# Performance work log

Measured on AMD Instinct MI355X. Metric: run time of the kernel, lower is better.

Reference implementation:

```python
import jax, jax.numpy as jnp
import numpy as np

LN_EPS = 1e-5


def setup_inputs() -> dict:
    key = jax.random.key(0)
    ks = jax.random.split(key, 10)
    B, T, D, K = 32, 1024, 512, 3
    enc = jax.random.normal(ks[0], (B, T, D), jnp.float32)
    dur = jax.random.randint(ks[1], (B, T), 0, 7, jnp.int32)
    s = 0.02
    return {
        "encoder_output": enc,
        "duration_target": dur,
        "conv1_w": jax.random.normal(ks[2], (K, D, D), jnp.float32) * s,  # HIO layout
        "conv1_b": jnp.zeros((D,), jnp.float32),
        "ln1_w": jnp.ones((D,), jnp.float32),
        "ln1_b": jnp.zeros((D,), jnp.float32),
        "conv2_w": jax.random.normal(ks[3], (K, D, D), jnp.float32) * s,
        "conv2_b": jnp.zeros((D,), jnp.float32),
        "ln2_w": jnp.ones((D,), jnp.float32),
        "ln2_b": jnp.zeros((D,), jnp.float32),
        "lin_w": jax.random.normal(ks[4], (D, 1), jnp.float32) * s,
        "lin_b": jnp.zeros((1,), jnp.float32),
        "max_len": 4096,
    }


def _conv_relu(x, w, b):
    # x: [B,T,D], w: [K, D_in, D_out] ('HIO'), 'SAME' padding == torch padding=1 for k=3
    y = jax.lax.conv_general_dilated(
        x, w, window_strides=(1,), padding="SAME",
        dimension_numbers=("NHC", "HIO", "NHC"))
    return jax.nn.relu(y + b)


def _layernorm(x, g, b):
    mu = jnp.mean(x, axis=-1, keepdims=True)
    var = jnp.mean(jnp.square(x - mu), axis=-1, keepdims=True)
    return (x - mu) * jax.lax.rsqrt(var + LN_EPS) * g + b


def reference(encoder_output, duration_target, conv1_w, conv1_b, ln1_w, ln1_b,
              conv2_w, conv2_b, ln2_w, ln2_b, lin_w, lin_b, max_len):
    B, T, D = encoder_output.shape
    # duration predictor: conv -> relu -> LN -> conv -> relu -> LN -> linear
    h = _layernorm(_conv_relu(encoder_output, conv1_w, conv1_b), ln1_w, ln1_b)
    h = _layernorm(_conv_relu(h, conv2_w, conv2_b), ln2_w, ln2_b)
    duration_predictor_output = (h @ lin_w + lin_b)[..., 0]  # [B,T]

    # training path: expand by duration_target via fused gather with cumulative offsets
    cum = jnp.cumsum(duration_target, axis=1)          # [B,T]
    pos = jnp.arange(max_len, dtype=jnp.int32)         # [L]
    # src index for output frame j: first t with cum[t] > j
    idx = jax.vmap(lambda c: jnp.searchsorted(c, pos, side="right"))(cum)  # [B,L]
    valid = pos[None, :] < cum[:, -1:]                  # [B,L]
    idx = jnp.minimum(idx, T - 1)
    expanded = jnp.take_along_axis(encoder_output, idx[:, :, None], axis=1)
    expanded = expanded * valid[:, :, None].astype(encoder_output.dtype)
    return expanded, duration_predictor_output
```

## Files before the change

kernel.cpp:

```cpp
#include <hip/hip_runtime.h>
#include <hip/hip_bf16.h>

#define BB 32
#define TT 1024
#define DD 512
#define LL 4096
#define KDIM 1536
#define TP 1026
#define ROWS (BB * TT)
#define NT (KDIM / 32)

typedef __attribute__((ext_vector_type(8))) short short8;
typedef __attribute__((ext_vector_type(8))) unsigned short ushort8;
typedef __attribute__((ext_vector_type(4))) float floatx4;

__device__ __forceinline__ unsigned short f2bf(float f) {
  unsigned int u = __builtin_bit_cast(unsigned int, f);
  u += 0x7FFF + ((u >> 16) & 1);
  return (unsigned short)(u >> 16);
}

#define GLOAD_LDS16(g, l)                                          \
  __builtin_amdgcn_global_load_lds(                                \
      (const __attribute__((address_space(1))) void*)(g),          \
      (__attribute__((address_space(3))) void*)(l), 16, 0, 0)

#define PAD_BLKS ((BB * TP) / 4)
#define W0 (PAD_BLKS + 16)
#define C0 (W0 + 384)
#define PREP_BLKS (C0 + 32)

__global__ __launch_bounds__(256) void prep_kernel(
    const float* __restrict__ X, unsigned short* __restrict__ Xp,
    unsigned short* __restrict__ Hp,
    const float* __restrict__ W1, unsigned short* __restrict__ Wt1,
    const float* __restrict__ W2, unsigned short* __restrict__ Wt2,
    const int* __restrict__ dur, int* __restrict__ cum,
    int* __restrict__ idx) {
  __shared__ float tile[64][65];
  const int tid = threadIdx.x;
  const int lane = tid & 63;

  if (blockIdx.x >= C0) {
    int* ls = reinterpret_cast<int*>(tile);
    const int b = blockIdx.x - C0;
    int4 v = reinterpret_cast<const int4*>(dur + b * TT)[tid];
    const int s0 = v.x, s1 = s0 + v.y, s2 = s1 + v.z, s3 = s2 + v.w;
    ls[tid] = s3;
    __syncthreads();
    for (int off = 1; off < 256; off <<= 1) {
      int x = (tid >= off) ? ls[tid - off] : 0;
      __syncthreads();
      ls[tid] += x;
      __syncthreads();
    }
    const int base = tid ? ls[tid - 1] : 0;
    int4 o = {base + s0, base + s1, base + s2, base + s3};
    reinterpret_cast<int4*>(cum + b * TT)[tid] = o;
    int* ib = idx + b * LL;
    int st = base;
    const int dv[4] = {v.x, v.y, v.z, v.w};
#pragma unroll
    for (int k = 0; k < 4; ++k) {
      const int e = min(st + dv[k], LL);
      for (int j = st; j < e; ++j) ib[j] = 4 * tid + k;
      st += dv[k];
    }
    return;
  }
  if (blockIdx.x >= W0) {
    const int w = blockIdx.x - W0;
    const int z = w / 192;
    const int rem = w - z * 192;
    const int bx = rem & 7;
    const int by = rem >> 3;
    const float* W = z ? W2 : W1;
    unsigned short* Wt = z ? Wt2 : Wt1;
    const int n0 = bx * 64;
    const int k0 = by * 64;
    const int c = lane;
    const int r4 = tid >> 6;
#pragma unroll
    for (int r = 0; r < 16; ++r)
      tile[r * 4 + r4][c] = W[(long)(k0 + r * 4 + r4) * DD + n0 + c];
    __syncthreads();
#pragma unroll
    for (int r = 0; r < 16; ++r)
      Wt[(long)(n0 + r * 4 + r4) * KDIM + k0 + c] = f2bf(tile[c][r * 4 + r4]);
    return;
  }
  if (blockIdx.x >= PAD_BLKS) {
    const int hid = (blockIdx.x - PAD_BLKS) * 4 + (tid >> 6);
    const int b = hid >> 1;
    const long r = (long)b * TP + ((hid & 1) ? (TP - 1) : 0);
    *reinterpret_cast<ushort8*>(Hp + r * DD + lane * 8) = (ushort8)0;
    return;
  }
  const int row = blockIdx.x * 4 + (tid >> 6);
  const int b  = row / TP;
  const int pr = row - b * TP;
  ushort8* o = reinterpret_cast<ushort8*>(Xp + (long)row * DD + lane * 8);
  ushort8 v;
  if (pr == 0 || pr == TP - 1) {
    v = (ushort8)0;
  } else {
    const float* p = X + ((long)(b * TT + pr - 1)) * DD + lane * 8;
    float4 a = *reinterpret_cast<const float4*>(p);
    float4 c = *reinterpret_cast<const float4*>(p + 4);
    v[0] = f2bf(a.x); v[1] = f2bf(a.y); v[2] = f2bf(a.z); v[3] = f2bf(a.w);
    v[4] = f2bf(c.x); v[5] = f2bf(c.y); v[6] = f2bf(c.z); v[7] = f2bf(c.w);
  }
  *o = v;
}

template <int LAYER>
__global__ __launch_bounds__(1024, 4) void fused_conv_ln_kernel(
    const unsigned short* __restrict__ Xp, const unsigned short* __restrict__ Wt,
    const float* __restrict__ bias, const float* __restrict__ g,
    const float* __restrict__ be, const float* __restrict__ lw,
    const float* __restrict__ lb, unsigned short* __restrict__ Hp,
    float* __restrict__ dpo) {
  __shared__ unsigned short As[3][128 * 32];
  __shared__ unsigned short Bs[3][512 * 32];
  __shared__ float sS[8][128];
  __shared__ float sQ[8][128];
  __shared__ float muL[128];
  __shared__ float rsL[128];

  const int tid  = threadIdx.x;
  const int lane = tid & 63;
  const int wid  = tid >> 6;
  const int srow = lane >> 2;
  const int gchunk = (lane & 3) ^ (srow & 3) ^ ((srow >> 2) & 3);
  const int frow = lane & 15;
  const int quad = lane >> 4;
  const int rdch = quad ^ (frow & 3) ^ ((frow >> 2) & 3);
  const int wm = (wid >> 3) * 64;
  const int wn = (wid & 7) * 64;
  const int wc = wid & 7;

  const int m0 = blockIdx.x * 128;
  const int bA = m0 >> 10;
  const int t0 = m0 & (TT - 1);

  const unsigned short* gA0 =
      Xp + (long)(bA * TP + t0 + (wid & 7) * 16 + srow) * DD + gchunk * 8;
  const int bb0 = (wid < 8) ? wid * 32 : 256 + (wid - 8) * 32;
  const unsigned short* gB0 =
      Wt + (long)(bb0 + srow) * KDIM + gchunk * 8;

  floatx4 acc[4][4];
#pragma unroll
  for (int i = 0; i < 4; ++i)
#pragma unroll
    for (int j = 0; j < 4; ++j) acc[i][j] = (floatx4){0.f, 0.f, 0.f, 0.f};

#define STAGE(bi, kk)                                                         \
  do {                                                                        \
    const int tap_ = (kk) >> 9;                                               \
    const int c0_  = (kk) & 511;                                              \
    if (wid < 8)                                                              \
      GLOAD_LDS16(gA0 + (long)tap_ * DD + c0_, &As[bi][(wid * 16) * 32]);     \
    GLOAD_LDS16(gB0 + (kk),                &Bs[bi][bb0 * 32]);                \
    GLOAD_LDS16(gB0 + (long)16 * KDIM + (kk), &Bs[bi][(bb0 + 16) * 32]);      \
  } while (0)

#define COMPUTE(bi)                                                           \
  do {                                                                        \
    short8 a_[4], b_[4];                                                      \
    _Pragma("unroll")                                                         \
    for (int i = 0; i < 4; ++i)                                               \
      a_[i] = *reinterpret_cast<const short8*>(                               \
          &As[bi][(wm + i * 16 + frow) * 32 + rdch * 8]);                     \
    _Pragma("unroll")                                                         \
    for (int j = 0; j < 4; ++j)                                               \
      b_[j] = *reinterpret_cast<const short8*>(                               \
          &Bs[bi][(wn + j * 16 + frow) * 32 + rdch * 8]);                     \
    _Pragma("unroll")                                                         \
    for (int i = 0; i < 4; ++i)                                               \
      _Pragma("unroll")                                                       \
      for (int j = 0; j < 4; ++j)                                             \
        acc[i][j] = __builtin_amdgcn_mfma_f32_16x16x32_bf16(                  \
            a_[i], b_[j], acc[i][j], 0, 0, 0);                                \
  } while (0)

  STAGE(0, 0);
  STAGE(1, 32);

  int cur = 0;
  int stg = 2;
  for (int t = 0; t < NT - 1; ++t) {
    if (wid < 8) asm volatile("s_waitcnt vmcnt(3)" ::: "memory");
    else         asm volatile("s_waitcnt vmcnt(2)" ::: "memory");
    __builtin_amdgcn_s_barrier();
    __builtin_amdgcn_sched_barrier(0);
    if (t + 2 < NT) STAGE(stg, (t + 2) * 32);
    COMPUTE(cur);
    cur = (cur == 2) ? 0 : cur + 1;
    stg = (stg == 2) ? 0 : stg + 1;
  }
  asm volatile("s_waitcnt vmcnt(0)" ::: "memory");
  __builtin_amdgcn_s_barrier();
  __builtin_amdgcn_sched_barrier(0);
  COMPUTE(cur);
#undef STAGE
#undef COMPUTE

  float bz[4];
#pragma unroll
  for (int j = 0; j < 4; ++j) bz[j] = bias[wn + j * 16 + frow];
#pragma unroll
  for (int i = 0; i < 4; ++i)
#pragma unroll
    for (int j = 0; j < 4; ++j)
#pragma unroll
      for (int r = 0; r < 4; ++r)
        acc[i][j][r] = fmaxf(acc[i][j][r] + bz[j], 0.f);

  float ps[16], pq[16];
#pragma unroll
  for (int i = 0; i < 4; ++i)
#pragma unroll
    for (int r = 0; r < 4; ++r) {
      float s = 0.f, q = 0.f;
#pragma unroll
      for (int j = 0; j < 4; ++j) {
        const float v = acc[i][j][r];
        s += v; q += v * v;
      }
      ps[i * 4 + r] = s; pq[i * 4 + r] = q;
    }
#pragma unroll
  for (int off = 1; off < 16; off <<= 1)
#pragma unroll
    for (int k = 0; k < 16; ++k) {
      ps[k] += __shfl_xor(ps[k], off);
      pq[k] += __shfl_xor(pq[k], off);
    }
  if (frow == 0) {
#pragma unroll
    for (int i = 0; i < 4; ++i)
#pragma unroll
      for (int r = 0; r < 4; ++r) {
        const int row = wm + i * 16 + quad * 4 + r;
        sS[wc][row] = ps[i * 4 + r];
        sQ[wc][row] = pq[i * 4 + r];
      }
  }
  __syncthreads();
  if (tid < 128) {
    float s = 0.f, q = 0.f;
#pragma unroll
    for (int c = 0; c < 8; ++c) { s += sS[c][tid]; q += sQ[c][tid]; }
    const float mu = s * (1.f / DD);
    const float var = q * (1.f / DD) - mu * mu;
    muL[tid] = mu;
    rsL[tid] = rsqrtf(var + 1e-5f);
  }
  __syncthreads();

  float gg[4], bb[4];
#pragma unroll
  for (int j = 0; j < 4; ++j) {
    gg[j] = g[wn + j * 16 + frow];
    bb[j] = be[wn + j * 16 + frow];
  }

  if constexpr (LAYER == 1) {
    unsigned short* Ls = &Bs[0][0];
    const int h = wm >> 6;
#pragma unroll
    for (int ph = 0; ph < 2; ++ph) {
      __syncthreads();
      if (h == ph) {
#pragma unroll
        for (int i = 0; i < 4; ++i)
#pragma unroll
          for (int r = 0; r < 4; ++r) {
            const int row = wm + i * 16 + quad * 4 + r;
            const float mu = muL[row];
            const float rs = rsL[row];
            const int lrow = row - ph * 64;
#pragma unroll
            for (int j = 0; j < 4; ++j) {
              const float v = (acc[i][j][r] - mu) * rs * gg[j] + bb[j];
              Ls[lrow * 520 + wn + j * 16 + frow] = f2bf(v);
            }
          }
      }
      __syncthreads();
      const long gbase = (long)(bA * TP + t0 + ph * 64 + 1) * DD;
#pragma unroll
      for (int it = 0; it < 4; ++it) {
        const int r2 = it * 16 + wid;
        const int cc = lane * 8;
        ushort8 val = *reinterpret_cast<const ushort8*>(&Ls[r2 * 520 + cc]);
        *reinterpret_cast<ushort8*>(&Hp[gbase + (long)r2 * DD + cc]) = val;
      }
    }
  } else {
    float ww[4];
#pragma unroll
    for (int j = 0; j < 4; ++j) ww[j] = lw[wn + j * 16 + frow];
#pragma unroll
    for (int i = 0; i < 4; ++i)
#pragma unroll
      for (int r = 0; r < 4; ++r) {
        const int row = wm + i * 16 + quad * 4 + r;
        const float mu = muL[row];
        const float rs = rsL[row];
        float d = 0.f;
#pragma unroll
        for (int j = 0; j < 4; ++j) {
          const float v = (acc[i][j][r] - mu) * rs * gg[j] + bb[j];
          d += v * ww[j];
        }
#pragma unroll
        for (int off = 1; off < 16; off <<= 1) d += __shfl_xor(d, off);
        if (frow == 0) sS[wc][row] = d;
      }
    __syncthreads();
    if (tid < 128) {
      float s = lb[0];
#pragma unroll
      for (int c = 0; c < 8; ++c) s += sS[c][tid];
      dpo[blockIdx.x * 128 + tid] = s;
    }
  }
}

__global__ __launch_bounds__(512) void gather_kernel(
    const float* __restrict__ X, const int* __restrict__ cum,
    const int* __restrict__ idx, float* __restrict__ out) {
  const long gf = (long)blockIdx.x * 4 + (threadIdx.x >> 7);
  const int tl = threadIdx.x & 127;
  const int b = (int)(gf >> 12);
  const int j = (int)(gf & (LL - 1));
  const int total = cum[b * TT + TT - 1];
  floatx4* o = reinterpret_cast<floatx4*>(out + gf * DD) + tl;
  if (j >= total) {
    *o = (floatx4){0.f, 0.f, 0.f, 0.f};
    return;
  }
  const int lo = idx[b * LL + j];
  const floatx4* src =
      reinterpret_cast<const floatx4*>(X + ((long)b * TT + lo) * DD) + tl;
  *o = *src;
}

extern "C" void kernel_launch(void* const* d_in, const int* in_sizes, int n_in,
                              void* d_out, int out_size, void* d_ws,
                              size_t ws_size, hipStream_t stream) {
  const float* enc = (const float*)d_in[0];
  const int* dur   = (const int*)d_in[1];
  const float* w1  = (const float*)d_in[2];
  const float* b1  = (const float*)d_in[3];
  const float* g1  = (const float*)d_in[4];
  const float* be1 = (const float*)d_in[5];
  const float* w2  = (const float*)d_in[6];
  const float* b2  = (const float*)d_in[7];
  const float* g2  = (const float*)d_in[8];
  const float* be2 = (const float*)d_in[9];
  const float* lw  = (const float*)d_in[10];
  const float* lb  = (const float*)d_in[11];

  float* out = (float*)d_out;
  float* expanded = out;
  float* dpo = out + (long)BB * LL * DD;

  unsigned short* enc_pad = (unsigned short*)(expanded);
  unsigned short* h1_pad  = (unsigned short*)(expanded + 9000000);
  unsigned short* wt1     = (unsigned short*)(expanded + 18000000);
  unsigned short* wt2     = (unsigned short*)(expanded + 18400000);
  int* cum = (int*)d_ws;
  int* idx = (int*)d_ws + ROWS;

  prep_kernel<<<PREP_BLKS, 256, 0, stream>>>(enc, enc_pad, h1_pad, w1, wt1,
                                             w2, wt2, dur, cum, idx);

  fused_conv_ln_kernel<1><<<ROWS / 128, 1024, 0, stream>>>(
      enc_pad, wt1, b1, g1, be1, nullptr, nullptr, h1_pad, nullptr);
  fused_conv_ln_kernel<2><<<ROWS / 128, 1024, 0, stream>>>(
      h1_pad, wt2, b2, g2, be2, lw, lb, nullptr, dpo);

  gather_kernel<<<BB * LL / 4, 512, 0, stream>>>(enc, cum, idx, expanded);
}
```

Before: 512.5 us.

## Load conv weight operand directly from global into registers, bypassing LDS staging

The weight (B) tiles are no longer staged into a triple-buffered LDS area. Each wave now reads its 64x32 weight fragment straight from global memory into registers every K step, and only the activation (A) tile still goes through LDS. The shared buffer is shrunk to a dedicated LayerNorm staging area, and the explicit vmcnt waits plus the peeled last iteration are removed. This cuts LDS traffic and shared-memory footprint. In exchange, global-load latency is exposed inside the main loop with no prefetch, and weight reads are duplicated across waves that share the same columns.

```diff
diff --git a/kernel.cpp b/kernel.cpp
--- a/kernel.cpp
+++ b/kernel.cpp
@@ -121,7 +121,7 @@
     const float* __restrict__ lb, unsigned short* __restrict__ Hp,
     float* __restrict__ dpo) {
   __shared__ unsigned short As[3][128 * 32];
-  __shared__ unsigned short Bs[3][512 * 32];
+  __shared__ unsigned short Ls[64 * 520];
   __shared__ float sS[8][128];
   __shared__ float sQ[8][128];
   __shared__ float muL[128];
@@ -144,10 +144,8 @@
   const int t0 = m0 & (TT - 1);
 
   const unsigned short* gA0 =
-      Xp + (long)(bA * TP + t0 + (wid & 7) * 16 + srow) * DD + gchunk * 8;
-  const int bb0 = (wid < 8) ? wid * 32 : 256 + (wid - 8) * 32;
-  const unsigned short* gB0 =
-      Wt + (long)(bb0 + srow) * KDIM + gchunk * 8;
+      Xp + (long)(bA * TP + t0 + wid * 16 + srow) * DD + gchunk * 8;
+  const unsigned short* gBW = Wt + (long)(wn + frow) * KDIM + quad * 8;
 
   floatx4 acc[4][4];
 #pragma unroll
@@ -161,50 +159,38 @@
     const int c0_  = (kk) & 511;                                              \
     if (wid < 8)                                                              \
       GLOAD_LDS16(gA0 + (long)tap_ * DD + c0_, &As[bi][(wid * 16) * 32]);     \
-    GLOAD_LDS16(gB0 + (kk),                &Bs[bi][bb0 * 32]);                \
-    GLOAD_LDS16(gB0 + (long)16 * KDIM + (kk), &Bs[bi][(bb0 + 16) * 32]);      \
-  } while (0)
-
-#define COMPUTE(bi)                                                           \
-  do {                                                                        \
-    short8 a_[4], b_[4];                                                      \
-    _Pragma("unroll")                                                         \
-    for (int i = 0; i < 4; ++i)                                               \
-      a_[i] = *reinterpret_cast<const short8*>(                               \
-          &As[bi][(wm + i * 16 + frow) * 32 + rdch * 8]);                     \
-    _Pragma("unroll")                                                         \
-    for (int j = 0; j < 4; ++j)                                               \
-      b_[j] = *reinterpret_cast<const short8*>(                               \
-          &Bs[bi][(wn + j * 16 + frow) * 32 + rdch * 8]);                     \
-    _Pragma("unroll")                                                         \
-    for (int i = 0; i < 4; ++i)                                               \
-      _Pragma("unroll")                                                       \
-      for (int j = 0; j < 4; ++j)                                             \
-        acc[i][j] = __builtin_amdgcn_mfma_f32_16x16x32_bf16(                  \
-            a_[i], b_[j], acc[i][j], 0, 0, 0);                                \
   } while (0)
 
   STAGE(0, 0);
   STAGE(1, 32);
+  if (wid < 8) asm volatile("s_waitcnt vmcnt(1)" ::: "memory");
 
   int cur = 0;
   int stg = 2;
-  for (int t = 0; t < NT - 1; ++t) {
-    if (wid < 8) asm volatile("s_waitcnt vmcnt(3)" ::: "memory");
-    else         asm volatile("s_waitcnt vmcnt(2)" ::: "memory");
+  for (int t = 0; t < NT; ++t) {
     __builtin_amdgcn_s_barrier();
     __builtin_amdgcn_sched_barrier(0);
+    const int k0 = t * 32;
+    short8 b_[4];
+#pragma unroll
+    for (int j = 0; j < 4; ++j)
+      b_[j] = *reinterpret_cast<const short8*>(gBW + (long)j * 16 * KDIM + k0);
     if (t + 2 < NT) STAGE(stg, (t + 2) * 32);
-    COMPUTE(cur);
+    short8 a_[4];
+#pragma unroll
+    for (int i = 0; i < 4; ++i)
+      a_[i] = *reinterpret_cast<const short8*>(
+          &As[cur][(wm + i * 16 + frow) * 32 + rdch * 8]);
+#pragma unroll
+    for (int i = 0; i < 4; ++i)
+#pragma unroll
+      for (int j = 0; j < 4; ++j)
+        acc[i][j] = __builtin_amdgcn_mfma_f32_16x16x32_bf16(
+            a_[i], b_[j], acc[i][j], 0, 0, 0);
     cur = (cur == 2) ? 0 : cur + 1;
     stg = (stg == 2) ? 0 : stg + 1;
   }
-  asm volatile("s_waitcnt vmcnt(0)" ::: "memory");
-  __builtin_amdgcn_s_barrier();
-  __builtin_amdgcn_sched_barrier(0);
-  COMPUTE(cur);
 #undef STAGE
-#undef COMPUTE
 
   float bz[4];
 #pragma unroll
@@ -267,7 +253,6 @@
   }
 
   if constexpr (LAYER == 1) {
-    unsigned short* Ls = &Bs[0][0];
     const int h = wm >> 6;
 #pragma unroll
     for (int ph = 0; ph < 2; ++ph) {
```

After: 604.9 us. +18.0%, slower.
